# Performance work log

Measured on AMD Instinct MI355X. Metric: run time of the kernel, lower is better.

The kernel has to match this reference:

```python
import jax, jax.numpy as jnp
import numpy as np

EPS = 1e-5  # eps placed on the diagonal via the 'eye' buffer in the torch module


def setup_inputs() -> dict:
    key = jax.random.key(0)
    k1, k2, k3 = jax.random.split(key, 3)
    B, C, H, W = 32, 256, 64, 64
    F = C // 4
    x = jax.random.normal(k1, (B, C, H, W), dtype=jnp.float32)
    # affine mixing weight [4,4,F] (torch inits diag(0.5,1,1,1); we add noise to exercise all paths)
    weight = jnp.eye(4, dtype=jnp.float32)[:, :, None] * jnp.ones((F,), jnp.float32) \
             + 0.1 * jax.random.normal(k2, (4, 4, F), dtype=jnp.float32)
    bias = 0.1 * jax.random.normal(k3, (4, F), dtype=jnp.float32)
    return {"x": x, "weight": weight, "bias": bias}


def reference(x, weight, bias):
    B, C, H, W = x.shape
    F = C // 4
    # split channels into 4 quaternion components: [4, B, F, H, W]
    xq = x.reshape(B, 4, F, H, W).transpose(1, 0, 2, 3, 4)
    # per (component, channel) mean over batch+spatial
    mean = xq.mean(axis=(1, 3, 4))                       # [4, F]
    xc = xq - mean[:, None, :, None, None]               # centered
    N = B * H * W
    # covariance across the 4 quaternion components, per channel: [F, 4, 4]
    v = xc.transpose(2, 0, 1, 3, 4).reshape(F, 4, N)     # [F, 4, N]
    cov = jnp.einsum('fin,fjn->fij', v, v) / N
    # batched 4x4 Cholesky and lower-triangular whitening solve
    L = jnp.linalg.cholesky(cov + EPS * jnp.eye(4, dtype=x.dtype))  # [F, 4, 4]
    z = jax.scipy.linalg.solve_triangular(L, v, lower=True)         # [F, 4, N]
    z = z.reshape(F, 4, B, H, W).transpose(1, 2, 0, 3, 4)           # [4, B, F, H, W]
    # unrolled 4x4 affine mix + bias, per channel
    out = jnp.einsum('ijf,jbfhw->ibfhw', weight, z) + bias[:, None, :, None, None]
    # re-concatenate components along channels -> [B, C, H, W]
    return out.transpose(1, 0, 2, 3, 4).reshape(B, C, H, W)
```

## Files before the change

### kernel.cpp

```cpp
#include <hip/hip_runtime.h>
#include <math.h>

constexpr int B   = 32;
constexpr int C   = 256;
constexpr int F   = 64;
constexpr int HW  = 64 * 64;
constexpr int HW4 = HW / 4;
constexpr int P4  = B * HW4;
constexpr float EPSV = 1e-5f;

constexpr int SBLOCKS = 32;
constexpr int SITER   = P4 / (SBLOCKS * 256);
constexpr int TBLOCKS = P4 / 256;

__global__ __launch_bounds__(256) void stats_kernel(const float* __restrict__ x,
                                                    float* __restrict__ sums) {
    const int f     = blockIdx.x / SBLOCKS;
    const int chunk = blockIdx.x % SBLOCKS;
    const int tid   = threadIdx.x;

    float acc[14];
#pragma unroll
    for (int i = 0; i < 14; ++i) acc[i] = 0.f;

    const float4* xb = reinterpret_cast<const float4*>(x);

#pragma unroll
    for (int it = 0; it < SITER; ++it) {
        const int p   = chunk * (256 * SITER) + it * 256 + tid;
        const int b   = p >> 10;
        const int hw4 = p & (HW4 - 1);
        float4 v[4];
#pragma unroll
        for (int q = 0; q < 4; ++q)
            v[q] = xb[(size_t)(b * C + q * F + f) * HW4 + hw4];
#pragma unroll
        for (int l = 0; l < 4; ++l) {
            float e0 = ((const float*)&v[0])[l];
            float e1 = ((const float*)&v[1])[l];
            float e2 = ((const float*)&v[2])[l];
            float e3 = ((const float*)&v[3])[l];
            acc[0] += e0; acc[1] += e1; acc[2] += e2; acc[3] += e3;
            acc[4]  += e0 * e0; acc[5]  += e0 * e1; acc[6]  += e0 * e2; acc[7]  += e0 * e3;
            acc[8]  += e1 * e1; acc[9]  += e1 * e2; acc[10] += e1 * e3;
            acc[11] += e2 * e2; acc[12] += e2 * e3;
            acc[13] += e3 * e3;
        }
    }

#pragma unroll
    for (int i = 0; i < 14; ++i) {
#pragma unroll
        for (int off = 32; off >= 1; off >>= 1)
            acc[i] += __shfl_down(acc[i], off, 64);
    }

    __shared__ float red[4][14];
    const int wave = tid >> 6;
    const int lane = tid & 63;
    if (lane == 0) {
#pragma unroll
        for (int i = 0; i < 14; ++i) red[wave][i] = acc[i];
    }
    __syncthreads();
    if (tid < 14) {
        float t = red[0][tid] + red[1][tid] + red[2][tid] + red[3][tid];
        atomicAdd(&sums[f * 14 + tid], t);
    }
}

__global__ __launch_bounds__(64) void solve_kernel(const float* __restrict__ sums,
                                                   const float* __restrict__ weight,
                                                   const float* __restrict__ bias,
                                                   float* __restrict__ Mc) {
    const int f = threadIdx.x;
    if (f >= F) return;
    const float invN = 1.0f / (float)(B * HW);

    float m[4];
#pragma unroll
    for (int q = 0; q < 4; ++q) m[q] = sums[f * 14 + q] * invN;

    float cov[4][4];
    {
        int k = 4;
        for (int i = 0; i < 4; ++i)
            for (int j = i; j < 4; ++j) {
                float cij = sums[f * 14 + k] * invN - m[i] * m[j];
                cov[i][j] = cij;
                cov[j][i] = cij;
                ++k;
            }
    }
#pragma unroll
    for (int i = 0; i < 4; ++i) cov[i][i] += EPSV;

    float L[4][4] = {};
    for (int i = 0; i < 4; ++i) {
        for (int j = 0; j <= i; ++j) {
            float s = cov[i][j];
            for (int k = 0; k < j; ++k) s -= L[i][k] * L[j][k];
            if (i == j) L[i][j] = sqrtf(s);
            else        L[i][j] = s / L[j][j];
        }
    }
    float Li[4][4] = {};
    for (int j = 0; j < 4; ++j) {
        Li[j][j] = 1.0f / L[j][j];
        for (int i = j + 1; i < 4; ++i) {
            float s = 0.f;
            for (int k = j; k < i; ++k) s += L[i][k] * Li[k][j];
            Li[i][j] = -s / L[i][i];
        }
    }
    float M[4][4];
    for (int i = 0; i < 4; ++i)
        for (int j = 0; j < 4; ++j) {
            float s = 0.f;
            for (int k = 0; k < 4; ++k)
                s += weight[(i * 4 + k) * F + f] * Li[k][j];
            M[i][j] = s;
        }
    for (int i = 0; i < 4; ++i) {
        float ci = bias[i * F + f];
        for (int j = 0; j < 4; ++j) ci -= M[i][j] * m[j];
#pragma unroll
        for (int j = 0; j < 4; ++j) Mc[f * 20 + i * 4 + j] = M[i][j];
        Mc[f * 20 + 16 + i] = ci;
    }
}

__global__ __launch_bounds__(256) void transform_kernel(const float* __restrict__ x,
                                                        const float* __restrict__ Mc,
                                                        float* __restrict__ out) {
    const int f     = blockIdx.x / TBLOCKS;
    const int chunk = blockIdx.x % TBLOCKS;

    __shared__ float sM[20];
    if (threadIdx.x < 20) sM[threadIdx.x] = Mc[f * 20 + threadIdx.x];
    __syncthreads();

    const int p   = chunk * 256 + threadIdx.x;
    const int b   = p >> 10;
    const int hw4 = p & (HW4 - 1);

    const float4* xb = reinterpret_cast<const float4*>(x);
    float4*       ob = reinterpret_cast<float4*>(out);

    float4 v[4];
#pragma unroll
    for (int q = 0; q < 4; ++q)
        v[q] = xb[(size_t)(b * C + q * F + f) * HW4 + hw4];

#pragma unroll
    for (int i = 0; i < 4; ++i) {
        const float m0 = sM[i * 4 + 0], m1 = sM[i * 4 + 1],
                    m2 = sM[i * 4 + 2], m3 = sM[i * 4 + 3];
        const float ci = sM[16 + i];
        float4 o;
        o.x = ci + m0 * v[0].x + m1 * v[1].x + m2 * v[2].x + m3 * v[3].x;
        o.y = ci + m0 * v[0].y + m1 * v[1].y + m2 * v[2].y + m3 * v[3].y;
        o.z = ci + m0 * v[0].z + m1 * v[1].z + m2 * v[2].z + m3 * v[3].z;
        o.w = ci + m0 * v[0].w + m1 * v[1].w + m2 * v[2].w + m3 * v[3].w;
        ob[(size_t)(b * C + i * F + f) * HW4 + hw4] = o;
    }
}

extern "C" void kernel_launch(void* const* d_in, const int* in_sizes, int n_in,
                              void* d_out, int out_size, void* d_ws, size_t ws_size,
                              hipStream_t stream) {
    const float* x      = (const float*)d_in[0];
    const float* weight = (const float*)d_in[1];
    const float* bias   = (const float*)d_in[2];
    float*       out    = (float*)d_out;

    float* sums = (float*)d_ws;
    float* Mc   = sums + F * 14;

    hipMemsetAsync(sums, 0, F * 14 * sizeof(float), stream);
    stats_kernel<<<F * SBLOCKS, 256, 0, stream>>>(x, sums);
    solve_kernel<<<1, 64, 0, stream>>>(sums, weight, bias, Mc);
    transform_kernel<<<F * TBLOCKS, 256, 0, stream>>>(x, Mc, out);
}
```

Before: 260.0 us.

## Fuse stats, solve and transform into one cooperative persistent kernel

```diff
diff --git a/kernel.cpp b/kernel.cpp
--- a/kernel.cpp
+++ b/kernel.cpp
@@ -1,5 +1,8 @@
 #include <hip/hip_runtime.h>
+#include <hip/hip_cooperative_groups.h>
 #include <math.h>
+
+namespace cg = cooperative_groups;
 
 constexpr int B   = 32;
 constexpr int C   = 256;
@@ -9,14 +12,180 @@
 constexpr int P4  = B * HW4;
 constexpr float EPSV = 1e-5f;
 
-constexpr int SBLOCKS = 32;
+constexpr int NBLK    = 1024;
+constexpr int SBLOCKS = NBLK / F;
 constexpr int SITER   = P4 / (SBLOCKS * 256);
-constexpr int TBLOCKS = P4 / 256;
+constexpr int TCHUNKS = P4 / 256;
+constexpr int TTOT    = F * TCHUNKS;
+
+typedef float f32x4 __attribute__((ext_vector_type(4)));
+
+__global__ __launch_bounds__(256, 4) void fused_kernel(
+    const float* __restrict__ x,
+    const float* __restrict__ weight,
+    const float* __restrict__ bias,
+    float* __restrict__ out,
+    float* __restrict__ sums)
+{
+    const int tid = threadIdx.x;
+    const int bid = blockIdx.x;
+    const float4* xb = reinterpret_cast<const float4*>(x);
+
+    __shared__ float red[4][14];
+    __shared__ float sMc[F][20];
+
+    {
+        const int f     = bid >> 4;
+        const int chunk = bid & (SBLOCKS - 1);
+
+        float acc[14];
+#pragma unroll
+        for (int i = 0; i < 14; ++i) acc[i] = 0.f;
+
+#pragma unroll
+        for (int it = 0; it < SITER; ++it) {
+            const int p   = chunk * (256 * SITER) + it * 256 + tid;
+            const int b   = p >> 10;
+            const int hw4 = p & (HW4 - 1);
+            float4 v[4];
+#pragma unroll
+            for (int q = 0; q < 4; ++q)
+                v[q] = xb[(size_t)(b * C + q * F + f) * HW4 + hw4];
+#pragma unroll
+            for (int l = 0; l < 4; ++l) {
+                float e0 = ((const float*)&v[0])[l];
+                float e1 = ((const float*)&v[1])[l];
+                float e2 = ((const float*)&v[2])[l];
+                float e3 = ((const float*)&v[3])[l];
+                acc[0] += e0; acc[1] += e1; acc[2] += e2; acc[3] += e3;
+                acc[4]  += e0 * e0; acc[5]  += e0 * e1; acc[6]  += e0 * e2; acc[7]  += e0 * e3;
+                acc[8]  += e1 * e1; acc[9]  += e1 * e2; acc[10] += e1 * e3;
+                acc[11] += e2 * e2; acc[12] += e2 * e3;
+                acc[13] += e3 * e3;
+            }
+        }
+
+#pragma unroll
+        for (int i = 0; i < 14; ++i) {
+#pragma unroll
+            for (int off = 32; off >= 1; off >>= 1)
+                acc[i] += __shfl_down(acc[i], off, 64);
+        }
+
+        const int wave = tid >> 6;
+        const int lane = tid & 63;
+        if (lane == 0) {
+#pragma unroll
+            for (int i = 0; i < 14; ++i) red[wave][i] = acc[i];
+        }
+        __syncthreads();
+        if (tid < 14) {
+            float t = red[0][tid] + red[1][tid] + red[2][tid] + red[3][tid];
+            atomicAdd(&sums[f * 14 + tid], t);
+        }
+    }
+
+    cg::this_grid().sync();
+
+    if (tid < F) {
+        const int f = tid;
+        const float invN = 1.0f / (float)(B * HW);
+
+        float s14[14];
+#pragma unroll
+        for (int i = 0; i < 14; ++i)
+            s14[i] = __hip_atomic_load(&sums[f * 14 + i], __ATOMIC_RELAXED,
+                                       __HIP_MEMORY_SCOPE_AGENT);
+
+        float m[4];
+#pragma unroll
+        for (int q = 0; q < 4; ++q) m[q] = s14[q] * invN;
+
+        float cov[4][4];
+        {
+            int k = 4;
+            for (int i = 0; i < 4; ++i)
+                for (int j = i; j < 4; ++j) {
+                    float cij = s14[k] * invN - m[i] * m[j];
+                    cov[i][j] = cij;
+                    cov[j][i] = cij;
+                    ++k;
+                }
+        }
+#pragma unroll
+        for (int i = 0; i < 4; ++i) cov[i][i] += EPSV;
+
+        float L[4][4] = {};
+        for (int i = 0; i < 4; ++i) {
+            for (int j = 0; j <= i; ++j) {
+                float s = cov[i][j];
+                for (int k = 0; k < j; ++k) s -= L[i][k] * L[j][k];
+                if (i == j) L[i][j] = sqrtf(s);
+                else        L[i][j] = s / L[j][j];
+            }
+        }
+        float Li[4][4] = {};
+        for (int j = 0; j < 4; ++j) {
+            Li[j][j] = 1.0f / L[j][j];
+            for (int i = j + 1; i < 4; ++i) {
+                float s = 0.f;
+                for (int k = j; k < i; ++k) s += L[i][k] * Li[k][j];
+                Li[i][j] = -s / L[i][i];
+            }
+        }
+        float M[4][4];
+        for (int i = 0; i < 4; ++i)
+            for (int j = 0; j < 4; ++j) {
+                float s = 0.f;
+                for (int k = 0; k < 4; ++k)
+                    s += weight[(i * 4 + k) * F + f] * Li[k][j];
+                M[i][j] = s;
+            }
+        for (int i = 0; i < 4; ++i) {
+            float ci = bias[i * F + f];
+            for (int j = 0; j < 4; ++j) ci -= M[i][j] * m[j];
+#pragma unroll
+            for (int j = 0; j < 4; ++j) sMc[f][i * 4 + j] = M[i][j];
+            sMc[f][16 + i] = ci;
+        }
+    }
+    __syncthreads();
+
+    f32x4* ob = reinterpret_cast<f32x4*>(out);
+    for (int c = bid; c < TTOT; c += NBLK) {
+        const int f   = c >> 7;
+        const int p   = ((c & (TCHUNKS - 1)) << 8) + tid;
+        const int b   = p >> 10;
+        const int hw4 = p & (HW4 - 1);
+
+        float4 v[4];
+#pragma unroll
+        for (int q = 0; q < 4; ++q)
+            v[q] = xb[(size_t)(b * C + q * F + f) * HW4 + hw4];
+
+#pragma unroll
+        for (int i = 0; i < 4; ++i) {
+            const float m0 = sMc[f][i * 4 + 0], m1 = sMc[f][i * 4 + 1],
+                        m2 = sMc[f][i * 4 + 2], m3 = sMc[f][i * 4 + 3];
+            const float ci = sMc[f][16 + i];
+            f32x4 o;
+            o.x = ci + m0 * v[0].x + m1 * v[1].x + m2 * v[2].x + m3 * v[3].x;
+            o.y = ci + m0 * v[0].y + m1 * v[1].y + m2 * v[2].y + m3 * v[3].y;
+            o.z = ci + m0 * v[0].z + m1 * v[1].z + m2 * v[2].z + m3 * v[3].z;
+            o.w = ci + m0 * v[0].w + m1 * v[1].w + m2 * v[2].w + m3 * v[3].w;
+            __builtin_nontemporal_store(o, &ob[(size_t)(b * C + i * F + f) * HW4 + hw4]);
+        }
+    }
+}
+
+constexpr int FB_SBLOCKS = 32;
+constexpr int FB_SITER   = P4 / (FB_SBLOCKS * 256);
+constexpr int FB_TBLOCKS = P4 / 256;
 
 __global__ __launch_bounds__(256) void stats_kernel(const float* __restrict__ x,
                                                     float* __restrict__ sums) {
-    const int f     = blockIdx.x / SBLOCKS;
-    const int chunk = blockIdx.x % SBLOCKS;
+    const int f     = blockIdx.x / FB_SBLOCKS;
+    const int chunk = blockIdx.x % FB_SBLOCKS;
     const int tid   = threadIdx.x;
 
     float acc[14];
@@ -26,8 +195,8 @@
     const float4* xb = reinterpret_cast<const float4*>(x);
 
 #pragma unroll
-    for (int it = 0; it < SITER; ++it) {
-        const int p   = chunk * (256 * SITER) + it * 256 + tid;
+    for (int it = 0; it < FB_SITER; ++it) {
+        const int p   = chunk * (256 * FB_SITER) + it * 256 + tid;
         const int b   = p >> 10;
         const int hw4 = p & (HW4 - 1);
         float4 v[4];
@@ -133,8 +302,8 @@
 __global__ __launch_bounds__(256) void transform_kernel(const float* __restrict__ x,
                                                         const float* __restrict__ Mc,
                                                         float* __restrict__ out) {
-    const int f     = blockIdx.x / TBLOCKS;
-    const int chunk = blockIdx.x % TBLOCKS;
+    const int f     = blockIdx.x / FB_TBLOCKS;
+    const int chunk = blockIdx.x % FB_TBLOCKS;
 
     __shared__ float sM[20];
     if (threadIdx.x < 20) sM[threadIdx.x] = Mc[f * 20 + threadIdx.x];
@@ -178,7 +347,14 @@
     float* Mc   = sums + F * 14;
 
     hipMemsetAsync(sums, 0, F * 14 * sizeof(float), stream);
-    stats_kernel<<<F * SBLOCKS, 256, 0, stream>>>(x, sums);
-    solve_kernel<<<1, 64, 0, stream>>>(sums, weight, bias, Mc);
-    transform_kernel<<<F * TBLOCKS, 256, 0, stream>>>(x, Mc, out);
-}
+
+    void* args[] = {(void*)&x, (void*)&weight, (void*)&bias, (void*)&out, (void*)&sums};
+    hipError_t err = hipLaunchCooperativeKernel((void*)fused_kernel,
+                                                dim3(NBLK), dim3(256),
+                                                args, 0, stream);
+    if (err != hipSuccess) {
+        stats_kernel<<<F * FB_SBLOCKS, 256, 0, stream>>>(x, sums);
+        solve_kernel<<<1, 64, 0, stream>>>(sums, weight, bias, Mc);
+        transform_kernel<<<F * FB_TBLOCKS, 256, 0, stream>>>(x, Mc, out);
+    }
+}
```

New measurement: 371.5 us. 42.9% more time.

## Fuse stats and solve kernels via last-block atomic counter; nontemporal output stores

Applied to the files above, without the earlier changes.

```diff
diff --git a/kernel.cpp b/kernel.cpp
--- a/kernel.cpp
+++ b/kernel.cpp
@@ -11,10 +11,19 @@
 
 constexpr int SBLOCKS = 32;
 constexpr int SITER   = P4 / (SBLOCKS * 256);
+constexpr int NSTAT   = F * SBLOCKS;
 constexpr int TBLOCKS = P4 / 256;
 
-__global__ __launch_bounds__(256) void stats_kernel(const float* __restrict__ x,
-                                                    float* __restrict__ sums) {
+typedef float f32x4 __attribute__((ext_vector_type(4)));
+
+__global__ __launch_bounds__(256) void stats_solve_kernel(
+    const float* __restrict__ x,
+    const float* __restrict__ weight,
+    const float* __restrict__ bias,
+    float* __restrict__ sums,
+    unsigned int* __restrict__ cnt,
+    float* __restrict__ Mc)
+{
     const int f     = blockIdx.x / SBLOCKS;
     const int chunk = blockIdx.x % SBLOCKS;
     const int tid   = threadIdx.x;
@@ -56,6 +65,7 @@
     }
 
     __shared__ float red[4][14];
+    __shared__ bool  s_last;
     const int wave = tid >> 6;
     const int lane = tid & 63;
     if (lane == 0) {
@@ -67,85 +77,100 @@
         float t = red[0][tid] + red[1][tid] + red[2][tid] + red[3][tid];
         atomicAdd(&sums[f * 14 + tid], t);
     }
+    __syncthreads();
+
+    if (tid == 0) {
+        __threadfence();
+        unsigned int old = atomicAdd(cnt, 1u);
+        s_last = (old == (unsigned)(NSTAT - 1));
+    }
+    __syncthreads();
+    if (!s_last) return;
+
+    __threadfence();
+    if (tid < F) {
+        const int ff = tid;
+        const float invN = 1.0f / (float)(B * HW);
+
+        float s14[14];
+#pragma unroll
+        for (int i = 0; i < 14; ++i)
+            s14[i] = __hip_atomic_load(&sums[ff * 14 + i], __ATOMIC_RELAXED,
+                                       __HIP_MEMORY_SCOPE_AGENT);
+
+        float m[4];
+#pragma unroll
+        for (int q = 0; q < 4; ++q) m[q] = s14[q] * invN;
+
+        float cov[4][4];
+        {
+            int k = 4;
+            for (int i = 0; i < 4; ++i)
+                for (int j = i; j < 4; ++j) {
+                    float cij = s14[k] * invN - m[i] * m[j];
+                    cov[i][j] = cij;
+                    cov[j][i] = cij;
+                    ++k;
+                }
+        }
+#pragma unroll
+        for (int i = 0; i < 4; ++i) cov[i][i] += EPSV;
+
+        float L[4][4] = {};
+        for (int i = 0; i < 4; ++i) {
+            for (int j = 0; j <= i; ++j) {
+                float s = cov[i][j];
+                for (int k = 0; k < j; ++k) s -= L[i][k] * L[j][k];
+                if (i == j) L[i][j] = sqrtf(s);
+                else        L[i][j] = s / L[j][j];
+            }
+        }
+        float Li[4][4] = {};
+        for (int j = 0; j < 4; ++j) {
+            Li[j][j] = 1.0f / L[j][j];
+            for (int i = j + 1; i < 4; ++i) {
+                float s = 0.f;
+                for (int k = j; k < i; ++k) s += L[i][k] * Li[k][j];
+                Li[i][j] = -s / L[i][i];
+            }
+        }
+        float M[4][4];
+        for (int i = 0; i < 4; ++i)
+            for (int j = 0; j < 4; ++j) {
+                float s = 0.f;
+                for (int k = 0; k < 4; ++k)
+                    s += weight[(i * 4 + k) * F + ff] * Li[k][j];
+                M[i][j] = s;
+            }
+        for (int i = 0; i < 4; ++i) {
+            float ci = bias[i * F + ff];
+            for (int j = 0; j < 4; ++j) ci -= M[i][j] * m[j];
+#pragma unroll
+            for (int j = 0; j < 4; ++j) Mc[ff * 20 + i * 4 + j] = M[i][j];
+            Mc[ff * 20 + 16 + i] = ci;
+        }
+    }
 }
 
-__global__ __launch_bounds__(64) void solve_kernel(const float* __restrict__ sums,
-                                                   const float* __restrict__ weight,
-                                                   const float* __restrict__ bias,
-                                                   float* __restrict__ Mc) {
-    const int f = threadIdx.x;
-    if (f >= F) return;
-    const float invN = 1.0f / (float)(B * HW);
-
-    float m[4];
-#pragma unroll
-    for (int q = 0; q < 4; ++q) m[q] = sums[f * 14 + q] * invN;
-
-    float cov[4][4];
-    {
-        int k = 4;
-        for (int i = 0; i < 4; ++i)
-            for (int j = i; j < 4; ++j) {
-                float cij = sums[f * 14 + k] * invN - m[i] * m[j];
-                cov[i][j] = cij;
-                cov[j][i] = cij;
-                ++k;
-            }
-    }
-#pragma unroll
-    for (int i = 0; i < 4; ++i) cov[i][i] += EPSV;
-
-    float L[4][4] = {};
-    for (int i = 0; i < 4; ++i) {
-        for (int j = 0; j <= i; ++j) {
-            float s = cov[i][j];
-            for (int k = 0; k < j; ++k) s -= L[i][k] * L[j][k];
-            if (i == j) L[i][j] = sqrtf(s);
-            else        L[i][j] = s / L[j][j];
-        }
-    }
-    float Li[4][4] = {};
-    for (int j = 0; j < 4; ++j) {
-        Li[j][j] = 1.0f / L[j][j];
-        for (int i = j + 1; i < 4; ++i) {
-            float s = 0.f;
-            for (int k = j; k < i; ++k) s += L[i][k] * Li[k][j];
-            Li[i][j] = -s / L[i][i];
-        }
-    }
-    float M[4][4];
-    for (int i = 0; i < 4; ++i)
-        for (int j = 0; j < 4; ++j) {
-            float s = 0.f;
-            for (int k = 0; k < 4; ++k)
-                s += weight[(i * 4 + k) * F + f] * Li[k][j];
-            M[i][j] = s;
-        }
-    for (int i = 0; i < 4; ++i) {
-        float ci = bias[i * F + f];
-        for (int j = 0; j < 4; ++j) ci -= M[i][j] * m[j];
-#pragma unroll
-        for (int j = 0; j < 4; ++j) Mc[f * 20 + i * 4 + j] = M[i][j];
-        Mc[f * 20 + 16 + i] = ci;
-    }
-}
-
-__global__ __launch_bounds__(256) void transform_kernel(const float* __restrict__ x,
-                                                        const float* __restrict__ Mc,
-                                                        float* __restrict__ out) {
-    const int f     = blockIdx.x / TBLOCKS;
-    const int chunk = blockIdx.x % TBLOCKS;
-
-    __shared__ float sM[20];
-    if (threadIdx.x < 20) sM[threadIdx.x] = Mc[f * 20 + threadIdx.x];
-    __syncthreads();
+__global__ __launch_bounds__(256) void transform_kernel(
+    const float* __restrict__ x,
+    const float* __restrict__ Mc,
+    float* __restrict__ out)
+{
+    const int f     = blockIdx.x >> 7;
+    const int chunk = blockIdx.x & (TBLOCKS - 1);
+
+    const float* mc = Mc + f * 20;
+    float mm[20];
+#pragma unroll
+    for (int i = 0; i < 20; ++i) mm[i] = mc[i];
 
     const int p   = chunk * 256 + threadIdx.x;
     const int b   = p >> 10;
     const int hw4 = p & (HW4 - 1);
 
     const float4* xb = reinterpret_cast<const float4*>(x);
-    float4*       ob = reinterpret_cast<float4*>(out);
+    f32x4*        ob = reinterpret_cast<f32x4*>(out);
 
     float4 v[4];
 #pragma unroll
@@ -154,15 +179,15 @@
 
 #pragma unroll
     for (int i = 0; i < 4; ++i) {
-        const float m0 = sM[i * 4 + 0], m1 = sM[i * 4 + 1],
-                    m2 = sM[i * 4 + 2], m3 = sM[i * 4 + 3];
-        const float ci = sM[16 + i];
-        float4 o;
+        const float m0 = mm[i * 4 + 0], m1 = mm[i * 4 + 1],
+                    m2 = mm[i * 4 + 2], m3 = mm[i * 4 + 3];
+        const float ci = mm[16 + i];
+        f32x4 o;
         o.x = ci + m0 * v[0].x + m1 * v[1].x + m2 * v[2].x + m3 * v[3].x;
         o.y = ci + m0 * v[0].y + m1 * v[1].y + m2 * v[2].y + m3 * v[3].y;
         o.z = ci + m0 * v[0].z + m1 * v[1].z + m2 * v[2].z + m3 * v[3].z;
         o.w = ci + m0 * v[0].w + m1 * v[1].w + m2 * v[2].w + m3 * v[3].w;
-        ob[(size_t)(b * C + i * F + f) * HW4 + hw4] = o;
+        __builtin_nontemporal_store(o, &ob[(size_t)(b * C + i * F + f) * HW4 + hw4]);
     }
 }
 
@@ -174,11 +199,12 @@
     const float* bias   = (const float*)d_in[2];
     float*       out    = (float*)d_out;
 
-    float* sums = (float*)d_ws;
-    float* Mc   = sums + F * 14;
-
-    hipMemsetAsync(sums, 0, F * 14 * sizeof(float), stream);
-    stats_kernel<<<F * SBLOCKS, 256, 0, stream>>>(x, sums);
-    solve_kernel<<<1, 64, 0, stream>>>(sums, weight, bias, Mc);
+    float*        sums = (float*)d_ws;
+    unsigned int* cnt  = (unsigned int*)(sums + F*14);
+    float*        Mc   = sums + F * 14 + 16;
+
+    hipMemsetAsync(sums, 0, (F * 14 + 16) * sizeof(float), stream);
+
+    stats_solve_kernel<<<NSTAT, 256, 0, stream>>>(x, weight, bias, sums, cnt, Mc);
     transform_kernel<<<F * TBLOCKS, 256, 0, stream>>>(x, Mc, out);
 }
```

Measured after the change: 353.1 us. 1.36x slower.
